# Optimization experiments

Hardware: AMD Instinct MI355X
Metric: run time of the kernel (lower is better)

The kernel has to match this reference:

```python
import jax, jax.numpy as jnp
import numpy as np
from jax import lax

NQ = 5  # qubits
NL = 3  # circuit layers


def conv2d(x, w, b):
    y = lax.conv_general_dilated(x, w, (1, 1), 'SAME',
                                 dimension_numbers=('NCHW', 'OIHW', 'NCHW'))
    return y + b[None, :, None, None]


def batchnorm(x, g, b, eps=1e-5):
    # training-mode batch statistics over (N,H,W), matching nn.BatchNorm2d in train()
    mu = x.mean((0, 2, 3), keepdims=True)
    var = x.var((0, 2, 3), keepdims=True)
    return g[None, :, None, None] * (x - mu) * lax.rsqrt(var + eps) + b[None, :, None, None]


def maxpool2(x):
    return lax.reduce_window(x, -jnp.inf, lax.max, (1, 1, 2, 2), (1, 1, 2, 2), 'VALID')


def _apply_1q(state, U, w):
    # state: (2,)*NQ, wire w is axis w (PennyLane default.qubit ordering)
    s = jnp.tensordot(U, state, axes=([1], [w]))
    return jnp.moveaxis(s, 0, w)


def _cnot(state, c, t):
    s0 = jnp.take(state, 0, axis=c)
    s1 = jnp.take(state, 1, axis=c)
    ta = t if t < c else t - 1
    s1 = jnp.flip(s1, axis=ta)  # X on target when control=1
    return jnp.stack([s0, s1], axis=c)


def _rx(t):
    c, s = jnp.cos(t / 2), jnp.sin(t / 2)
    return jnp.array([[c, -1j * s], [-1j * s, c]], dtype=jnp.complex64)


def _ry(t):
    c, s = jnp.cos(t / 2), jnp.sin(t / 2)
    return jnp.array([[c, -s], [s, c]], dtype=jnp.complex64)


def _rz(t):
    e = jnp.exp(-1j * t / 2)
    z = jnp.zeros((), jnp.complex64)
    return jnp.array([[e, z], [z, jnp.conj(e)]], dtype=jnp.complex64)


def quantum_circuit(inputs, weights):
    # inputs: (5,), weights: (30,)  -> scalar <Z0 Z1 Z2>
    state = jnp.zeros((2,) * NQ, jnp.complex64).at[(0,) * NQ].set(1.0)
    npl = NQ * 2  # weights per layer = 10
    nw = weights.shape[0]
    for l in range(NL):
        for i in range(NQ):
            state = _apply_1q(state, _rx(inputs[i]), i)
        for i in range(NQ):
            state = _apply_1q(state, _ry(weights[(l * npl + i) % nw]), i)
            state = _apply_1q(state, _rz(weights[(l * npl + i + NQ) % nw]), i)
        for i in range(NQ - 1):
            state = _cnot(state, i, i + 1)
        state = _cnot(state, NQ - 1, 0)
    probs = jnp.abs(state) ** 2
    z = jnp.array([1.0, -1.0], jnp.float32)
    sign = z[:, None, None] * z[None, :, None] * z[None, None, :]  # Z on wires 0,1,2
    return jnp.sum(probs * sign[:, :, :, None, None])


def setup_inputs() -> dict:
    key = jax.random.key(0)
    ks = jax.random.split(key, 12)
    d = {}
    d['x'] = jax.random.normal(ks[0], (256, 1, 224, 224), jnp.float32)
    d['conv1_w'] = jax.random.normal(ks[1], (16, 1, 3, 3), jnp.float32) * 0.1
    d['conv1_b'] = jnp.zeros((16,), jnp.float32)
    d['bn1_g'] = jnp.ones((16,), jnp.float32)
    d['bn1_b'] = jnp.zeros((16,), jnp.float32)
    d['conv2_w'] = jax.random.normal(ks[2], (32, 16, 3, 3), jnp.float32) * 0.05
    d['conv2_b'] = jnp.zeros((32,), jnp.float32)
    d['bn2_g'] = jnp.ones((32,), jnp.float32)
    d['bn2_b'] = jnp.zeros((32,), jnp.float32)
    d['conv3_w'] = jax.random.normal(ks[3], (64, 32, 3, 3), jnp.float32) * 0.05
    d['conv3_b'] = jnp.zeros((64,), jnp.float32)
    d['bn3_g'] = jnp.ones((64,), jnp.float32)
    d['bn3_b'] = jnp.zeros((64,), jnp.float32)
    d['fc1_w'] = jax.random.normal(ks[4], (64, 5), jnp.float32) * 0.1   # (in,out)
    d['fc1_b'] = jnp.zeros((5,), jnp.float32)
    d['ln_g'] = jnp.ones((5,), jnp.float32)
    d['ln_b'] = jnp.zeros((5,), jnp.float32)
    d['q_params'] = jax.random.uniform(ks[5], (30,), jnp.float32)
    d['fc2_w'] = jax.random.normal(ks[6], (1, 32), jnp.float32) * 0.5
    d['fc2_b'] = jnp.zeros((32,), jnp.float32)
    d['fc3_w'] = jax.random.normal(ks[7], (32, 2), jnp.float32) * 0.2
    d['fc3_b'] = jnp.zeros((2,), jnp.float32)
    return d


def reference(x, conv1_w, conv1_b, bn1_g, bn1_b, conv2_w, conv2_b, bn2_g, bn2_b,
              conv3_w, conv3_b, bn3_g, bn3_b, fc1_w, fc1_b, ln_g, ln_b,
              q_params, fc2_w, fc2_b, fc3_w, fc3_b):
    h = maxpool2(jax.nn.relu(batchnorm(conv2d(x, conv1_w, conv1_b), bn1_g, bn1_b)))
    h = maxpool2(jax.nn.relu(batchnorm(conv2d(h, conv2_w, conv2_b), bn2_g, bn2_b)))
    h = maxpool2(jax.nn.relu(batchnorm(conv2d(h, conv3_w, conv3_b), bn3_g, bn3_b)))
    # dropout is identity in eval; adaptive avg pool (1,1) + flatten
    h = h.mean((2, 3))                    # (B, 64)
    h = h @ fc1_w + fc1_b                 # (B, 5)
    mu = h.mean(-1, keepdims=True)
    var = h.var(-1, keepdims=True)
    h = ln_g * (h - mu) * lax.rsqrt(var + 1e-5) + ln_b
    q = jax.vmap(lambda inp: quantum_circuit(inp, q_params))(h)  # (B,)
    q = q[:, None].astype(jnp.float32)    # (B, 1)
    h2 = jax.nn.relu(q @ fc2_w + fc2_b)   # (B, 32)
    logits = h2 @ fc3_w + fc3_b           # (B, 2)
    return jax.nn.log_softmax(logits, axis=1)
```

## Files before the change

kernel.cpp:

```cpp
#include <hip/hip_runtime.h>
#include <hip/hip_bf16.h>


typedef _Float16 f16;
typedef _Float16 f16x2 __attribute__((ext_vector_type(2)));
typedef _Float16 f16x4 __attribute__((ext_vector_type(4)));
typedef _Float16 f16x8 __attribute__((ext_vector_type(8)));
typedef float f32x4 __attribute__((ext_vector_type(4)));
typedef float f32x16 __attribute__((ext_vector_type(16)));

#define DEV static __device__ __forceinline__

DEV float wave_sum(float v) {
#pragma unroll
  for (int off = 32; off > 0; off >>= 1) v += __shfl_xor(v, off, 64);
  return v;
}

__global__ __launch_bounds__(256) void repack(const float* __restrict__ w2,
                                              const float* __restrict__ w3,
                                              f16* __restrict__ Bt2,
                                              f16* __restrict__ Bt3) {
  int t = blockIdx.x * 256 + threadIdx.x;
  int T = gridDim.x * 256;
  for (int i = t; i < 32 * 168; i += T) {
    int oc = i / 168, kk = i - oc * 168;
    float v = 0.f;
    if (kk < 144) {
      int tap = kk >> 4, ic = kk & 15;
      v = w2[(oc * 16 + ic) * 9 + tap];
    }
    Bt2[i] = (f16)v;
  }
  for (int i = t; i < 64 * 296; i += T) {
    int oc = i / 296, kk = i - oc * 296;
    float v = 0.f;
    if (kk < 288) {
      int tap = kk / 32, ic = kk & 31;
      v = w3[(oc * 32 + ic) * 9 + tap];
    }
    Bt3[i] = (f16)v;
  }
}

__global__ __launch_bounds__(64) void finalize(const float* __restrict__ banks,
                                               const float* __restrict__ g,
                                               const float* __restrict__ b,
                                               float* __restrict__ scsh, int C,
                                               float inv_n) {
  int c = blockIdx.x, bk = threadIdx.x;
  float s = banks[bk * 2 * C + c];
  float qq = banks[bk * 2 * C + C + c];
  s = wave_sum(s);
  qq = wave_sum(qq);
  if (bk == 0) {
    float mean = s * inv_n;
    float var = qq * inv_n - mean * mean;
    float sc = g[c] * rsqrtf(var + 1e-5f);
    scsh[c] = sc;
    scsh[C + c] = b[c] - mean * sc;
  }
}

__global__ __launch_bounds__(256) void l1_mfma32(const float* __restrict__ x,
                                                 const float* __restrict__ w1,
                                                 float* __restrict__ banks,
                                                 f16* __restrict__ h1raw) {
  __shared__ f16 xA[18 * 240];
  __shared__ f16 xB[18 * 240];
  __shared__ f16 lrow[4 * 3616];
  __shared__ float lstat[32];
  int bid = blockIdx.x;
  int n = bid / 14, band = bid - n * 14;
  int y0 = band * 16;
  int t = threadIdx.x;
  if (t < 32) lstat[t] = 0.f;
  for (int i = t; i < 1008; i += 256) {
    int r = i / 56, k = i - r * 56;
    int y = y0 - 1 + r;
    float4 v = make_float4(0.f, 0.f, 0.f, 0.f);
    if ((unsigned)y < 224u)
      v = *(const float4*)(x + ((size_t)(n * 224 + y)) * 224 + k * 4);
    f16 h0 = (f16)v.x, h1 = (f16)v.y, h2 = (f16)v.z, h3 = (f16)v.w;
    f16* pa = xA + r * 240 + 4 * k + 1;
    pa[0] = h0; pa[1] = h1; pa[2] = h2; pa[3] = h3;
    f16x4 pk = {h0, h1, h2, h3};
    *(f16x4*)(xB + r * 240 + 4 * k) = pk;
  }
  if (t < 18) {
    xA[t * 240 + 0] = (f16)0.f;
    xA[t * 240 + 225] = (f16)0.f;
    xA[t * 240 + 226] = (f16)0.f;
    xB[t * 240 + 224] = (f16)0.f;
    xB[t * 240 + 225] = (f16)0.f;
  }
  __syncthreads();

  int wave = t >> 6, lane = t & 63;
  int g = lane >> 5, m32 = lane & 31;
  int oc = m32 & 15, s = m32 >> 4;

  f16x8 b;
#pragma unroll
  for (int j = 0; j < 8; j++) {
    int ky = 2 * g + (j >> 2), kx = j & 3;
    int kys = ky - s;
    float wv = 0.f;
    if (kx < 3 && kys >= 0 && kys < 3) wv = w1[oc * 9 + kys * 3 + kx];
    b[j] = (f16)wv;
  }

  const f16* abase = (m32 & 1) ? (xB + (m32 - 1)) : (xA + m32);
  f16* myrow = lrow + wave * 3616;
  f16* mrow = myrow + s * 1808;
  f32x16 zero16;
#pragma unroll
  for (int r = 0; r < 16; r++) zero16[r] = 0.f;
  const int bp[8] = {0, 1, 4, 5, 8, 9, 12, 13};
  float ssum = 0.f, ssq = 0.f;

  for (int rp = wave; rp < 8; rp += 4) {
    int r0 = 2 * rp + 2 * g;
    const f16* rbase = abase + r0 * 240;
#pragma unroll
    for (int xt = 0; xt < 7; xt++) {
      const f16* p0 = rbase + xt * 32;
      f16x2 v0 = *(const f16x2*)(p0);
      f16x2 v1 = *(const f16x2*)(p0 + 2);
      f16x2 v2 = *(const f16x2*)(p0 + 240);
      f16x2 v3 = *(const f16x2*)(p0 + 242);
      f16x8 a = {v0[0], v0[1], v1[0], v1[1], v2[0], v2[1], v3[0], v3[1]};
      f32x16 acc = __builtin_amdgcn_mfma_f32_32x32x16_f16(a, b, zero16, 0, 0, 0);
#pragma unroll
      for (int r = 0; r < 16; r++) {
        float v = acc[r];
        ssum += v;
        ssq += v * v;
      }
#pragma unroll
      for (int i = 0; i < 8; i++) {
        float pm = fmaxf(acc[2 * i], acc[2 * i + 1]);
        int pxp = xt * 16 + bp[i] + 2 * g;
        mrow[pxp * 16 + oc] = (f16)pm;
      }
    }
    int ph = band * 8 + rp;
    f16* gdst = h1raw + ((size_t)(n * 112) + ph) * 112 * 16;
    for (int i = lane; i < 224; i += 64) {
      f16x8 va = *(const f16x8*)(myrow + i * 8);
      f16x8 vb = *(const f16x8*)(myrow + 1808 + i * 8);
#pragma unroll
      for (int k = 0; k < 8; k++) va[k] = (va[k] > vb[k]) ? va[k] : vb[k];
      *(f16x8*)(gdst + i * 8) = va;
    }
  }
  ssum += __shfl_xor(ssum, 16, 64);
  ssum += __shfl_xor(ssum, 32, 64);
  ssq += __shfl_xor(ssq, 16, 64);
  ssq += __shfl_xor(ssq, 32, 64);
  if (lane < 16) {
    atomicAdd(&lstat[oc], ssum);
    atomicAdd(&lstat[16 + oc], ssq);
  }
  __syncthreads();
  if (t < 32) atomicAdd(&banks[(bid & 63) * 32 + t], lstat[t]);
}

__global__ __launch_bounds__(256) void l2_gemm(const f16* __restrict__ h1,
                                               const f16* __restrict__ Btg,
                                               const float* __restrict__ scsh1,
                                               f16* __restrict__ p2,
                                               float* __restrict__ banks) {
  extern __shared__ char smem[];
  f16* lin = (f16*)smem;
  float* lstat = (float*)(smem + 32832);
  f16* lpool = (f16*)smem;
  int bid = blockIdx.x;
  int n = bid / 28, band = bid - n * 28, h0 = band * 4;
  int t = threadIdx.x;
  int wave = t >> 6, lane = t & 63, q = lane >> 4, wi = lane & 15;
  const int icq = (q & 1) * 8;
  f16x8 breg0[5], breg1[5];
#pragma unroll
  for (int j = 0; j < 5; j++) {
    breg0[j] = *(const f16x8*)(Btg + wi * 168 + j * 32 + q * 8);
    breg1[j] = *(const f16x8*)(Btg + (16 + wi) * 168 + j * 32 + q * 8);
  }
  if (t < 64) lstat[t] = 0.f;
  {
    for (int i = t; i < 1344; i += 256) {
      int r = i / 224, c = i - r * 224;
      int y = h0 + r - 1;
      f16x8 o = {0, 0, 0, 0, 0, 0, 0, 0};
      if ((unsigned)y < 112u) {
        f16x8 xv =
            *(const f16x8*)(h1 + ((size_t)(n * 112 + y)) * 112 * 16 + c * 8);
        int ch0 = (c & 1) * 8;
#pragma unroll
        for (int k = 0; k < 8; k++) {
          float f = (float)xv[k] * scsh1[ch0 + k] + scsh1[16 + ch0 + k];
          o[k] = (f16)fmaxf(f, 0.f);
        }
      }
      *(f16x8*)(lin + (r * 114 + 1 + (c >> 1)) * 24 + (c & 1) * 8) = o;
    }
    if (t < 24) {
      int r = t >> 2, k = t & 3;
      f16x8 z = {0, 0, 0, 0, 0, 0, 0, 0};
      int pos = (k < 2) ? 0 : 113;
      *(f16x8*)(lin + (r * 114 + pos) * 24 + (k & 1) * 8) = z;
    }
  }
  __syncthreads();
  f32x4 acc[7][2];
#pragma unroll
  for (int f = 0; f < 7; f++)
#pragma unroll
    for (int nf = 0; nf < 2; nf++)
#pragma unroll
      for (int r = 0; r < 4; r++) acc[f][nf][r] = 0.f;

#pragma unroll
  for (int j = 0; j < 5; j++) {
    const int tA = 2 * j, tB = 2 * j + 1;
    const int kyA = tA / 3, kxA = tA % 3;
    const int kyB = (tB < 9) ? tB / 3 : 0, kxB = (tB < 9) ? tB % 3 : 0;
    bool hiq = (q >= 2);
    int ky = hiq ? kyB : kyA;
    int kx = hiq ? kxB : kxA;
    const f16* aptr0 = lin + ((wave + ky) * 114 + wi + kx) * 24 + icq;
    f16x8 b0 = breg0[j];
    f16x8 b1 = breg1[j];
#pragma unroll
    for (int f = 0; f < 7; f++) {
      f16x8 a = *(const f16x8*)(aptr0 + f * 384);
      acc[f][0] = __builtin_amdgcn_mfma_f32_16x16x32_f16(a, b0, acc[f][0], 0, 0, 0);
      acc[f][1] = __builtin_amdgcn_mfma_f32_16x16x32_f16(a, b1, acc[f][1], 0, 0, 0);
    }
  }
  float s0 = 0.f, q0 = 0.f, s1 = 0.f, q1 = 0.f;
#pragma unroll
  for (int f = 0; f < 7; f++)
#pragma unroll
    for (int r = 0; r < 4; r++) {
      float v0 = acc[f][0][r], v1 = acc[f][1][r];
      s0 += v0; q0 += v0 * v0;
      s1 += v1; q1 += v1 * v1;
    }
  s0 += __shfl_xor(s0, 16, 64); s0 += __shfl_xor(s0, 32, 64);
  q0 += __shfl_xor(q0, 16, 64); q0 += __shfl_xor(q0, 32, 64);
  s1 += __shfl_xor(s1, 16, 64); s1 += __shfl_xor(s1, 32, 64);
  q1 += __shfl_xor(q1, 16, 64); q1 += __shfl_xor(q1, 32, 64);
  if (q == 0) {
    atomicAdd(&lstat[wi], s0);
    atomicAdd(&lstat[16 + wi], s1);
    atomicAdd(&lstat[32 + wi], q0);
    atomicAdd(&lstat[48 + wi], q1);
  }
  __syncthreads();
  if (wave & 1) {
#pragma unroll
    for (int f = 0; f < 7; f++)
#pragma unroll
      for (int nf = 0; nf < 2; nf++) {
        int ch = nf * 16 + wi;
        int pc0 = f * 8 + q * 2;
        float m0 = fmaxf(acc[f][nf][0], acc[f][nf][1]);
        float m1 = fmaxf(acc[f][nf][2], acc[f][nf][3]);
        lpool[((wave >> 1) * 56 + pc0) * 32 + ch] = (f16)m0;
        lpool[((wave >> 1) * 56 + pc0 + 1) * 32 + ch] = (f16)m1;
      }
  }
  __syncthreads();
  if (!(wave & 1)) {
    int ph = band * 2 + (wave >> 1);
#pragma unroll
    for (int f = 0; f < 7; f++)
#pragma unroll
      for (int nf = 0; nf < 2; nf++) {
        int ch = nf * 16 + wi;
        int pc0 = f * 8 + q * 2;
        float m0 = fmaxf(acc[f][nf][0], acc[f][nf][1]);
        float m1 = fmaxf(acc[f][nf][2], acc[f][nf][3]);
        m0 = fmaxf(m0, (float)lpool[((wave >> 1) * 56 + pc0) * 32 + ch]);
        m1 = fmaxf(m1, (float)lpool[((wave >> 1) * 56 + pc0 + 1) * 32 + ch]);
        size_t ob = (((size_t)n * 56 + ph) * 56) * 32;
        p2[ob + (size_t)pc0 * 32 + ch] = (f16)m0;
        p2[ob + (size_t)(pc0 + 1) * 32 + ch] = (f16)m1;
      }
  }
  if (t < 64) {
    int i = t >> 5, c = t & 31;
    atomicAdd(&banks[(bid & 63) * 64 + i * 32 + c], lstat[i * 32 + c]);
  }
}

__global__ __launch_bounds__(256) void l3_gemm(const f16* __restrict__ p2,
                                               const f16* __restrict__ Btg,
                                               const float* __restrict__ scsh2,
                                               f16* __restrict__ p3,
                                               float* __restrict__ banks) {
  extern __shared__ char smem[];
  f16* lin = (f16*)smem;
  float* lstat = (float*)(smem + 27840);
  f16* lpool = (f16*)smem;
  int bx = blockIdx.x;
  int n = bx / 14, band = bx - n * 14, h0 = band * 4;
  int t = threadIdx.x;
  int wave = t >> 6, lane = t & 63, q = lane >> 4, wi = lane & 15;
  int mhalf = wave & 1, nfpair = wave >> 1;
  f16x8 breg0[9], breg1[9];
#pragma unroll
  for (int j = 0; j < 9; j++) {
    breg0[j] = *(const f16x8*)(Btg + (nfpair * 32 + wi) * 296 + j * 32 + q * 8);
    breg1[j] =
        *(const f16x8*)(Btg + (nfpair * 32 + 16 + wi) * 296 + j * 32 + q * 8);
  }
  if (t < 128) lstat[t] = 0.f;
  {
    for (int i = t; i < 1344; i += 256) {
      int r = i / 224, rem = i - r * 224;
      int c = rem >> 2, cp = rem & 3;
      int y = h0 + r - 1;
      f16x8 o = {0, 0, 0, 0, 0, 0, 0, 0};
      if ((unsigned)y < 56u) {
        const f16* src = p2 + (((size_t)(n * 56 + y)) * 56 + c) * 32 + cp * 8;
        f16x8 xv = *(const f16x8*)src;
        int ch0 = cp * 8;
#pragma unroll
        for (int k = 0; k < 8; k++) {
          float f = (float)xv[k] * scsh2[ch0 + k] + scsh2[32 + ch0 + k];
          o[k] = (f16)fmaxf(f, 0.f);
        }
      }
      *(f16x8*)(lin + (r * 58 + 1 + c) * 40 + cp * 8) = o;
    }
    if (t < 48) {
      int r = t / 8, k = t & 7;
      int col = (k < 4) ? 0 : 57, cp = k & 3;
      f16x8 z = {0, 0, 0, 0, 0, 0, 0, 0};
      *(f16x8*)(lin + (r * 58 + col) * 40 + cp * 8) = z;
    }
  }
  __syncthreads();
  int abase[7];
#pragma unroll
  for (int f = 0; f < 7; f++) {
    int pos = mhalf * 112 + f * 16 + wi;
    int r = pos / 56, w = pos - r * 56;
    abase[f] = (r * 58 + w) * 40 + q * 8;
  }
  f32x4 acc[7][2];
#pragma unroll
  for (int f = 0; f < 7; f++)
#pragma unroll
    for (int nf = 0; nf < 2; nf++)
#pragma unroll
      for (int r = 0; r < 4; r++) acc[f][nf][r] = 0.f;

#pragma unroll
  for (int j = 0; j < 9; j++) {
    const int ky = j / 3, kx = j % 3;
    f16x8 b0 = breg0[j];
    f16x8 b1 = breg1[j];
#pragma unroll
    for (int f = 0; f < 7; f++) {
      f16x8 a = *(const f16x8*)(lin + abase[f] + (ky * 58 + kx) * 40);
      acc[f][0] = __builtin_amdgcn_mfma_f32_16x16x32_f16(a, b0, acc[f][0], 0, 0, 0);
      acc[f][1] = __builtin_amdgcn_mfma_f32_16x16x32_f16(a, b1, acc[f][1], 0, 0, 0);
    }
  }
  int ch0 = nfpair * 32 + wi, ch1 = ch0 + 16;
  float s0 = 0.f, q0 = 0.f, s1 = 0.f, q1 = 0.f;
#pragma unroll
  for (int f = 0; f < 7; f++)
#pragma unroll
    for (int r = 0; r < 4; r++) {
      float v0 = acc[f][0][r], v1 = acc[f][1][r];
      s0 += v0; q0 += v0 * v0;
      s1 += v1; q1 += v1 * v1;
    }
  s0 += __shfl_xor(s0, 16, 64); s0 += __shfl_xor(s0, 32, 64);
  q0 += __shfl_xor(q0, 16, 64); q0 += __shfl_xor(q0, 32, 64);
  s1 += __shfl_xor(s1, 16, 64); s1 += __shfl_xor(s1, 32, 64);
  q1 += __shfl_xor(q1, 16, 64); q1 += __shfl_xor(q1, 32, 64);
  if (q == 0) {
    atomicAdd(&lstat[ch0], s0);
    atomicAdd(&lstat[ch1], s1);
    atomicAdd(&lstat[64 + ch0], q0);
    atomicAdd(&lstat[64 + ch1], q1);
  }
  __syncthreads();
#pragma unroll
  for (int f = 0; f < 7; f++) {
    int pos = mhalf * 112 + f * 16 + q * 4;
    int r0 = pos / 56, w0 = pos - r0 * 56;
#pragma unroll
    for (int nf = 0; nf < 2; nf++) {
      int ch = nf ? ch1 : ch0;
      float m0 = fmaxf(acc[f][nf][0], acc[f][nf][1]);
      float m1 = fmaxf(acc[f][nf][2], acc[f][nf][3]);
      lpool[(r0 * 28 + (w0 >> 1)) * 64 + ch] = (f16)m0;
      lpool[(r0 * 28 + (w0 >> 1) + 1) * 64 + ch] = (f16)m1;
    }
  }
  __syncthreads();
  for (int i = t; i < 3584; i += 256) {
    int ch = i & 63, rest = i >> 6;
    int pc = rest % 28, pr = rest / 28;
    float v = fmaxf((float)lpool[((2 * pr) * 28 + pc) * 64 + ch],
                    (float)lpool[((2 * pr + 1) * 28 + pc) * 64 + ch]);
    int gpr = band * 2 + pr;
    p3[(((size_t)n * 28 + gpr) * 28 + pc) * 64 + ch] = (f16)v;
  }
  if (t < 128) {
    atomicAdd(&banks[(bx & 63) * 128 + t], lstat[t]);
  }
}

__global__ __launch_bounds__(256) void head_pool(
    const f16* __restrict__ p3, const float* __restrict__ scsh3,
    const float* __restrict__ fc1w, const float* __restrict__ fc1b,
    float* __restrict__ featg) {
  int n = blockIdx.x, t = threadIdx.x;
  __shared__ float red[64 * 33];
  __shared__ float meanc[64];
  int oct = t & 7, strip = t >> 3;
  float sc[8], sh[8];
#pragma unroll
  for (int k = 0; k < 8; k++) {
    sc[k] = scsh3[oct * 8 + k];
    sh[k] = scsh3[64 + oct * 8 + k];
  }
  float acc[8];
#pragma unroll
  for (int k = 0; k < 8; k++) acc[k] = 0.f;
  const f16* base = p3 + (size_t)n * 50176 + oct * 8;
  for (int px = strip; px < 784; px += 32) {
    f16x8 v = *(const f16x8*)(base + (size_t)px * 64);
#pragma unroll
    for (int k = 0; k < 8; k++)
      acc[k] += fmaxf((float)v[k] * sc[k] + sh[k], 0.f);
  }
#pragma unroll
  for (int k = 0; k < 8; k++) red[(oct * 8 + k) * 33 + strip] = acc[k];
  __syncthreads();
  if (t < 64) {
    float s = 0.f;
    for (int j = 0; j < 32; j++) s += red[t * 33 + j];
    meanc[t] = s * (1.f / 784.f);
  }
  __syncthreads();
  if (t < 5) {
    float a = fc1b[t];
    for (int i = 0; i < 64; i++) a += meanc[i] * fc1w[i * 5 + t];
    featg[n * 8 + t] = a;
  }
}

template <int W>
DEV void g_rx(float (&sr)[32], float (&si)[32], float c, float s) {
  constexpr int m = 1 << (4 - W);
#pragma unroll
  for (int i0 = 0; i0 < 32; i0++)
    if (!(i0 & m)) {
      int i1 = i0 | m;
      float a0r = sr[i0], a0i = si[i0], a1r = sr[i1], a1i = si[i1];
      sr[i0] = c * a0r + s * a1i;
      si[i0] = c * a0i - s * a1r;
      sr[i1] = s * a0i + c * a1r;
      si[i1] = -s * a0r + c * a1i;
    }
}

template <int W>
DEV void g_ry(float (&sr)[32], float (&si)[32], float c, float s) {
  constexpr int m = 1 << (4 - W);
#pragma unroll
  for (int i0 = 0; i0 < 32; i0++)
    if (!(i0 & m)) {
      int i1 = i0 | m;
      float a0r = sr[i0], a0i = si[i0], a1r = sr[i1], a1i = si[i1];
      sr[i0] = c * a0r - s * a1r;
      si[i0] = c * a0i - s * a1i;
      sr[i1] = s * a0r + c * a1r;
      si[i1] = s * a0i + c * a1i;
    }
}

template <int W>
DEV void g_rz(float (&sr)[32], float (&si)[32], float c, float s) {
  constexpr int m = 1 << (4 - W);
#pragma unroll
  for (int i0 = 0; i0 < 32; i0++)
    if (!(i0 & m)) {
      int i1 = i0 | m;
      float a0r = sr[i0], a0i = si[i0], a1r = sr[i1], a1i = si[i1];
      sr[i0] = c * a0r + s * a0i;
      si[i0] = c * a0i - s * a0r;
      sr[i1] = c * a1r - s * a1i;
      si[i1] = c * a1i + s * a1r;
    }
}

template <int C, int T>
DEV void g_cnot(float (&sr)[32], float (&si)[32]) {
  constexpr int mc = 1 << (4 - C), mt = 1 << (4 - T);
#pragma unroll
  for (int i0 = 0; i0 < 32; i0++)
    if ((i0 & mc) && !(i0 & mt)) {
      int i1 = i0 | mt;
      float tr = sr[i0]; sr[i0] = sr[i1]; sr[i1] = tr;
      float ti = si[i0]; si[i0] = si[i1]; si[i1] = ti;
    }
}

__global__ __launch_bounds__(64) void head_q(
    const float* __restrict__ featg, const float* __restrict__ lng,
    const float* __restrict__ lnb, const float* __restrict__ qp,
    const float* __restrict__ fc2w, const float* __restrict__ fc2b,
    const float* __restrict__ fc3w, const float* __restrict__ fc3b,
    float* __restrict__ out) {
  int n = blockIdx.x * 64 + threadIdx.x;
  float f[5];
#pragma unroll
  for (int i = 0; i < 5; i++) f[i] = featg[n * 8 + i];
  float mu = (f[0] + f[1] + f[2] + f[3] + f[4]) * 0.2f;
  float var = 0.f;
#pragma unroll
  for (int i = 0; i < 5; i++) { float d = f[i] - mu; var += d * d; }
  var *= 0.2f;
  float inv = rsqrtf(var + 1e-5f);
#pragma unroll
  for (int i = 0; i < 5; i++) f[i] = lng[i] * (f[i] - mu) * inv + lnb[i];

  float cx[5], sx[5];
#pragma unroll
  for (int i = 0; i < 5; i++) {
    cx[i] = cosf(0.5f * f[i]);
    sx[i] = sinf(0.5f * f[i]);
  }
  float sr[32], si[32];
#pragma unroll
  for (int i = 0; i < 32; i++) { sr[i] = 0.f; si[i] = 0.f; }
  sr[0] = 1.f;

  for (int l = 0; l < 3; l++) {
    g_rx<0>(sr, si, cx[0], sx[0]);
    g_rx<1>(sr, si, cx[1], sx[1]);
    g_rx<2>(sr, si, cx[2], sx[2]);
    g_rx<3>(sr, si, cx[3], sx[3]);
    g_rx<4>(sr, si, cx[4], sx[4]);
#define WIRE_YZ(I)                                             \
  {                                                            \
    float ty = qp[l * 10 + I];                                 \
    g_ry<I>(sr, si, cosf(0.5f * ty), sinf(0.5f * ty));         \
    float tz = qp[l * 10 + I + 5];                             \
    g_rz<I>(sr, si, cosf(0.5f * tz), sinf(0.5f * tz));         \
  }
    WIRE_YZ(0) WIRE_YZ(1) WIRE_YZ(2) WIRE_YZ(3) WIRE_YZ(4)
#undef WIRE_YZ
    g_cnot<0, 1>(sr, si);
    g_cnot<1, 2>(sr, si);
    g_cnot<2, 3>(sr, si);
    g_cnot<3, 4>(sr, si);
    g_cnot<4, 0>(sr, si);
  }
  float qv = 0.f;
#pragma unroll
  for (int idx = 0; idx < 32; idx++) {
    float p = sr[idx] * sr[idx] + si[idx] * si[idx];
    qv += (__popc(idx & 0x1C) & 1) ? -p : p;
  }
  float l0 = fc3b[0], l1 = fc3b[1];
  for (int j = 0; j < 32; j++) {
    float hv = fmaxf(qv * fc2w[j] + fc2b[j], 0.f);
    l0 += hv * fc3w[j * 2];
    l1 += hv * fc3w[j * 2 + 1];
  }
  float mx = fmaxf(l0, l1);
  float lse = mx + logf(expf(l0 - mx) + expf(l1 - mx));
  out[n * 2 + 0] = l0 - lse;
  out[n * 2 + 1] = l1 - lse;
}

extern "C" void kernel_launch(void* const* d_in, const int* in_sizes, int n_in,
                              void* d_out, int out_size, void* d_ws,
                              size_t ws_size, hipStream_t stream) {
  const float* x    = (const float*)d_in[0];
  const float* w1   = (const float*)d_in[1];
  const float* bn1g = (const float*)d_in[3];
  const float* bn1b = (const float*)d_in[4];
  const float* w2   = (const float*)d_in[5];
  const float* bn2g = (const float*)d_in[7];
  const float* bn2b = (const float*)d_in[8];
  const float* w3   = (const float*)d_in[9];
  const float* bn3g = (const float*)d_in[11];
  const float* bn3b = (const float*)d_in[12];
  const float* fc1w = (const float*)d_in[13];
  const float* fc1b = (const float*)d_in[14];
  const float* lng  = (const float*)d_in[15];
  const float* lnb  = (const float*)d_in[16];
  const float* qp   = (const float*)d_in[17];
  const float* fc2w = (const float*)d_in[18];
  const float* fc2b = (const float*)d_in[19];
  const float* fc3w = (const float*)d_in[20];
  const float* fc3b = (const float*)d_in[21];
  float* out = (float*)d_out;

  char* ws = (char*)d_ws;
  float* banks1 = (float*)ws;
  float* banks2 = (float*)(ws + 8192);
  float* banks3 = (float*)(ws + 24576);
  float* scsh1 = (float*)(ws + 57344);
  float* scsh2 = (float*)(ws + 57472);
  float* scsh3 = (float*)(ws + 57728);
  f16* Bt2 = (f16*)(ws + 58240);
  f16* Bt3 = (f16*)(ws + 68992);
  f16* h1 = (f16*)(ws + 106880);
  f16* p2 = (f16*)(ws + 106880 + 102760448ULL);
  f16* p3 = (f16*)(ws + 106880 + 102760448ULL + 51380224ULL);
  float* featg = banks2;

  hipMemsetAsync(ws, 0, 57344, stream);
  repack<<<16, 256, 0, stream>>>(w2, w3, Bt2, Bt3);
  l1_mfma32<<<3584, 256, 0, stream>>>(x, w1, banks1, h1);
  finalize<<<16, 64, 0, stream>>>(banks1, bn1g, bn1b, scsh1, 16,
                                  1.f / 12845056.f);
  l2_gemm<<<7168, 256, 33088, stream>>>(h1, Bt2, scsh1, p2, banks2);
  finalize<<<32, 64, 0, stream>>>(banks2, bn2g, bn2b, scsh2, 32,
                                  1.f / 3211264.f);
  l3_gemm<<<3584, 256, 28352, stream>>>(p2, Bt3, scsh2, p3, banks3);
  finalize<<<64, 64, 0, stream>>>(banks3, bn3g, bn3b, scsh3, 64,
                                  1.f / 802816.f);
  head_pool<<<256, 256, 0, stream>>>(p3, scsh3, fc1w, fc1b, featg);
  head_q<<<4, 64, 0, stream>>>(featg, lng, lnb, qp, fc2w, fc2b, fc3w, fc3b,
                               out);
}
```

Baseline: 367.2 us.

## Make l2_gemm persistent over four bands with double-buffered LDS prefetch

Each l2_gemm block now handles four consecutive 4-row bands instead of one, cutting the grid from 7168 to 1792 blocks. The block prefetches the next band's input into registers and writes it to a second LDS buffer while the current band's MFMAs run. BN statistics accumulate across bands before one atomic flush, which reduces per-block setup, B-fragment loads and atomics. The cost is higher LDS use (about 73KB) and register pressure under launch_bounds(256,2), which lowers occupancy, and one extra barrier per band.

```diff
diff --git a/kernel.cpp b/kernel.cpp
--- a/kernel.cpp
+++ b/kernel.cpp
@@ -166,129 +166,211 @@
   if (t < 32) atomicAdd(&banks[(bid & 63) * 32 + t], lstat[t]);
 }
 
-__global__ __launch_bounds__(256) void l2_gemm(const f16* __restrict__ h1,
-                                               const f16* __restrict__ Btg,
-                                               const float* __restrict__ scsh1,
-                                               f16* __restrict__ p2,
-                                               float* __restrict__ banks) {
+__global__ __launch_bounds__(256, 2) void l2_gemm(
+    const f16* __restrict__ h1, const f16* __restrict__ Btg,
+    const float* __restrict__ scsh1, f16* __restrict__ p2,
+    float* __restrict__ banks) {
   extern __shared__ char smem[];
-  f16* lin = (f16*)smem;
-  float* lstat = (float*)(smem + 32832);
-  f16* lpool = (f16*)smem;
+  f16* lin0 = (f16*)smem;
+  f16* lin1 = (f16*)(smem + 32832);
+  f16* lpool = (f16*)(smem + 65664);
+  float* lstat = (float*)(smem + 72832);
   int bid = blockIdx.x;
-  int n = bid / 28, band = bid - n * 28, h0 = band * 4;
+  int n = bid / 7, sb = bid - n * 7;
   int t = threadIdx.x;
   int wave = t >> 6, lane = t & 63, q = lane >> 4, wi = lane & 15;
   const int icq = (q & 1) * 8;
+
   f16x8 breg0[5], breg1[5];
 #pragma unroll
   for (int j = 0; j < 5; j++) {
     breg0[j] = *(const f16x8*)(Btg + wi * 168 + j * 32 + q * 8);
     breg1[j] = *(const f16x8*)(Btg + (16 + wi) * 168 + j * 32 + q * 8);
   }
+
+  f16x8 L[6];
+  {
+    int gb4 = sb * 16;
+#pragma unroll
+    for (int k = 0; k < 6; k++) {
+      int i = t + k * 256;
+      f16x8 v = {0, 0, 0, 0, 0, 0, 0, 0};
+      if (i < 1344) {
+        int r = i / 224, c = i - r * 224;
+        int y = gb4 + r - 1;
+        if ((unsigned)y < 112u)
+          v = *(const f16x8*)(h1 + ((size_t)(n * 112 + y)) * 112 * 16 + c * 8);
+      }
+      L[k] = v;
+    }
+  }
+  __builtin_amdgcn_sched_barrier(0);
   if (t < 64) lstat[t] = 0.f;
+  if (t < 48) {
+    f16* dst = (t < 24) ? lin0 : lin1;
+    int tt = (t < 24) ? t : t - 24;
+    int r = tt >> 2, k2 = tt & 3;
+    f16x8 z = {0, 0, 0, 0, 0, 0, 0, 0};
+    int pos = (k2 < 2) ? 0 : 113;
+    *(f16x8*)(dst + (r * 114 + pos) * 24 + (k2 & 1) * 8) = z;
+  }
   {
-    for (int i = t; i < 1344; i += 256) {
-      int r = i / 224, c = i - r * 224;
-      int y = h0 + r - 1;
-      f16x8 o = {0, 0, 0, 0, 0, 0, 0, 0};
-      if ((unsigned)y < 112u) {
-        f16x8 xv =
-            *(const f16x8*)(h1 + ((size_t)(n * 112 + y)) * 112 * 16 + c * 8);
-        int ch0 = (c & 1) * 8;
-#pragma unroll
-        for (int k = 0; k < 8; k++) {
-          float f = (float)xv[k] * scsh1[ch0 + k] + scsh1[16 + ch0 + k];
-          o[k] = (f16)fmaxf(f, 0.f);
+    int gb4 = sb * 16;
+#pragma unroll
+    for (int k = 0; k < 6; k++) {
+      int i = t + k * 256;
+      if (i < 1344) {
+        int r = i / 224, c = i - r * 224;
+        int y = gb4 + r - 1;
+        f16x8 o = {0, 0, 0, 0, 0, 0, 0, 0};
+        if ((unsigned)y < 112u) {
+          f16x8 xv = L[k];
+          int ch0 = (c & 1) * 8;
+#pragma unroll
+          for (int e = 0; e < 8; e++) {
+            float f = (float)xv[e] * scsh1[ch0 + e] + scsh1[16 + ch0 + e];
+            o[e] = (f16)fmaxf(f, 0.f);
+          }
         }
-      }
-      *(f16x8*)(lin + (r * 114 + 1 + (c >> 1)) * 24 + (c & 1) * 8) = o;
-    }
-    if (t < 24) {
-      int r = t >> 2, k = t & 3;
-      f16x8 z = {0, 0, 0, 0, 0, 0, 0, 0};
-      int pos = (k < 2) ? 0 : 113;
-      *(f16x8*)(lin + (r * 114 + pos) * 24 + (k & 1) * 8) = z;
-    }
-  }
-  __syncthreads();
-  f32x4 acc[7][2];
-#pragma unroll
-  for (int f = 0; f < 7; f++)
-#pragma unroll
-    for (int nf = 0; nf < 2; nf++)
-#pragma unroll
-      for (int r = 0; r < 4; r++) acc[f][nf][r] = 0.f;
-
-#pragma unroll
-  for (int j = 0; j < 5; j++) {
-    const int tA = 2 * j, tB = 2 * j + 1;
-    const int kyA = tA / 3, kxA = tA % 3;
-    const int kyB = (tB < 9) ? tB / 3 : 0, kxB = (tB < 9) ? tB % 3 : 0;
-    bool hiq = (q >= 2);
-    int ky = hiq ? kyB : kyA;
-    int kx = hiq ? kxB : kxA;
-    const f16* aptr0 = lin + ((wave + ky) * 114 + wi + kx) * 24 + icq;
-    f16x8 b0 = breg0[j];
-    f16x8 b1 = breg1[j];
-#pragma unroll
-    for (int f = 0; f < 7; f++) {
-      f16x8 a = *(const f16x8*)(aptr0 + f * 384);
-      acc[f][0] = __builtin_amdgcn_mfma_f32_16x16x32_f16(a, b0, acc[f][0], 0, 0, 0);
-      acc[f][1] = __builtin_amdgcn_mfma_f32_16x16x32_f16(a, b1, acc[f][1], 0, 0, 0);
-    }
-  }
-  float s0 = 0.f, q0 = 0.f, s1 = 0.f, q1 = 0.f;
-#pragma unroll
-  for (int f = 0; f < 7; f++)
-#pragma unroll
-    for (int r = 0; r < 4; r++) {
-      float v0 = acc[f][0][r], v1 = acc[f][1][r];
-      s0 += v0; q0 += v0 * v0;
-      s1 += v1; q1 += v1 * v1;
-    }
-  s0 += __shfl_xor(s0, 16, 64); s0 += __shfl_xor(s0, 32, 64);
-  q0 += __shfl_xor(q0, 16, 64); q0 += __shfl_xor(q0, 32, 64);
-  s1 += __shfl_xor(s1, 16, 64); s1 += __shfl_xor(s1, 32, 64);
-  q1 += __shfl_xor(q1, 16, 64); q1 += __shfl_xor(q1, 32, 64);
+        *(f16x8*)(lin0 + (r * 114 + 1 + (c >> 1)) * 24 + (c & 1) * 8) = o;
+      }
+    }
+  }
+  __syncthreads();
+
+  float tS0 = 0.f, tQ0 = 0.f, tS1 = 0.f, tQ1 = 0.f;
+  f16* cur = lin0;
+  f16* nxt = lin1;
+
+  for (int b = 0; b < 4; b++) {
+    int gb = sb * 4 + b;
+    if (b < 3) {
+      int gb4 = (gb + 1) * 4;
+#pragma unroll
+      for (int k = 0; k < 6; k++) {
+        int i = t + k * 256;
+        f16x8 v = {0, 0, 0, 0, 0, 0, 0, 0};
+        if (i < 1344) {
+          int r = i / 224, c = i - r * 224;
+          int y = gb4 + r - 1;
+          if ((unsigned)y < 112u)
+            v = *(const f16x8*)(h1 +
+                                ((size_t)(n * 112 + y)) * 112 * 16 + c * 8);
+        }
+        L[k] = v;
+      }
+      __builtin_amdgcn_sched_barrier(0);
+    }
+
+    f32x4 acc[7][2];
+#pragma unroll
+    for (int f = 0; f < 7; f++)
+#pragma unroll
+      for (int nf = 0; nf < 2; nf++)
+#pragma unroll
+        for (int r = 0; r < 4; r++) acc[f][nf][r] = 0.f;
+
+#pragma unroll
+    for (int j = 0; j < 5; j++) {
+      const int tA = 2 * j, tB = 2 * j + 1;
+      const int kyA = tA / 3, kxA = tA % 3;
+      const int kyB = (tB < 9) ? tB / 3 : 0, kxB = (tB < 9) ? tB % 3 : 0;
+      bool hiq = (q >= 2);
+      int ky = hiq ? kyB : kyA;
+      int kx = hiq ? kxB : kxA;
+      const f16* aptr0 = cur + ((wave + ky) * 114 + wi + kx) * 24 + icq;
+      f16x8 b0 = breg0[j];
+      f16x8 b1 = breg1[j];
+#pragma unroll
+      for (int f = 0; f < 7; f++) {
+        f16x8 a = *(const f16x8*)(aptr0 + f * 384);
+        acc[f][0] =
+            __builtin_amdgcn_mfma_f32_16x16x32_f16(a, b0, acc[f][0], 0, 0, 0);
+        acc[f][1] =
+            __builtin_amdgcn_mfma_f32_16x16x32_f16(a, b1, acc[f][1], 0, 0, 0);
+      }
+    }
+
+#pragma unroll
+    for (int f = 0; f < 7; f++)
+#pragma unroll
+      for (int r = 0; r < 4; r++) {
+        float v0 = acc[f][0][r], v1 = acc[f][1][r];
+        tS0 += v0; tQ0 += v0 * v0;
+        tS1 += v1; tQ1 += v1 * v1;
+      }
+
+    if (wave & 1) {
+#pragma unroll
+      for (int f = 0; f < 7; f++)
+#pragma unroll
+        for (int nf = 0; nf < 2; nf++) {
+          int ch = nf * 16 + wi;
+          int pc0 = f * 8 + q * 2;
+          float m0 = fmaxf(acc[f][nf][0], acc[f][nf][1]);
+          float m1 = fmaxf(acc[f][nf][2], acc[f][nf][3]);
+          lpool[((wave >> 1) * 56 + pc0) * 32 + ch] = (f16)m0;
+          lpool[((wave >> 1) * 56 + pc0 + 1) * 32 + ch] = (f16)m1;
+        }
+    }
+
+    if (b < 3) {
+      int gb4 = (gb + 1) * 4;
+#pragma unroll
+      for (int k = 0; k < 6; k++) {
+        int i = t + k * 256;
+        if (i < 1344) {
+          int r = i / 224, c = i - r * 224;
+          int y = gb4 + r - 1;
+          f16x8 o = {0, 0, 0, 0, 0, 0, 0, 0};
+          if ((unsigned)y < 112u) {
+            f16x8 xv = L[k];
+            int ch0 = (c & 1) * 8;
+#pragma unroll
+            for (int e = 0; e < 8; e++) {
+              float f = (float)xv[e] * scsh1[ch0 + e] + scsh1[16 + ch0 + e];
+              o[e] = (f16)fmaxf(f, 0.f);
+            }
+          }
+          *(f16x8*)(nxt + (r * 114 + 1 + (c >> 1)) * 24 + (c & 1) * 8) = o;
+        }
+      }
+    }
+    __syncthreads();
+
+    if (!(wave & 1)) {
+      int ph = gb * 2 + (wave >> 1);
+#pragma unroll
+      for (int f = 0; f < 7; f++)
+#pragma unroll
+        for (int nf = 0; nf < 2; nf++) {
+          int ch = nf * 16 + wi;
+          int pc0 = f * 8 + q * 2;
+          float m0 = fmaxf(acc[f][nf][0], acc[f][nf][1]);
+          float m1 = fmaxf(acc[f][nf][2], acc[f][nf][3]);
+          m0 = fmaxf(m0, (float)lpool[((wave >> 1) * 56 + pc0) * 32 + ch]);
+          m1 = fmaxf(m1, (float)lpool[((wave >> 1) * 56 + pc0 + 1) * 32 + ch]);
+          size_t ob = (((size_t)n * 56 + ph) * 56) * 32;
+          p2[ob + (size_t)pc0 * 32 + ch] = (f16)m0;
+          p2[ob + (size_t)(pc0 + 1) * 32 + ch] = (f16)m1;
+        }
+    }
+    __syncthreads();
+
+    f16* tmpp = cur; cur = nxt; nxt = tmpp;
+  }
+
+  tS0 += __shfl_xor(tS0, 16, 64); tS0 += __shfl_xor(tS0, 32, 64);
+  tQ0 += __shfl_xor(tQ0, 16, 64); tQ0 += __shfl_xor(tQ0, 32, 64);
+  tS1 += __shfl_xor(tS1, 16, 64); tS1 += __shfl_xor(tS1, 32, 64);
+  tQ1 += __shfl_xor(tQ1, 16, 64); tQ1 += __shfl_xor(tQ1, 32, 64);
   if (q == 0) {
-    atomicAdd(&lstat[wi], s0);
-    atomicAdd(&lstat[16 + wi], s1);
-    atomicAdd(&lstat[32 + wi], q0);
-    atomicAdd(&lstat[48 + wi], q1);
-  }
-  __syncthreads();
-  if (wave & 1) {
-#pragma unroll
-    for (int f = 0; f < 7; f++)
-#pragma unroll
-      for (int nf = 0; nf < 2; nf++) {
-        int ch = nf * 16 + wi;
-        int pc0 = f * 8 + q * 2;
-        float m0 = fmaxf(acc[f][nf][0], acc[f][nf][1]);
-        float m1 = fmaxf(acc[f][nf][2], acc[f][nf][3]);
-        lpool[((wave >> 1) * 56 + pc0) * 32 + ch] = (f16)m0;
-        lpool[((wave >> 1) * 56 + pc0 + 1) * 32 + ch] = (f16)m1;
-      }
-  }
-  __syncthreads();
-  if (!(wave & 1)) {
-    int ph = band * 2 + (wave >> 1);
-#pragma unroll
-    for (int f = 0; f < 7; f++)
-#pragma unroll
-      for (int nf = 0; nf < 2; nf++) {
-        int ch = nf * 16 + wi;
-        int pc0 = f * 8 + q * 2;
-        float m0 = fmaxf(acc[f][nf][0], acc[f][nf][1]);
-        float m1 = fmaxf(acc[f][nf][2], acc[f][nf][3]);
-        m0 = fmaxf(m0, (float)lpool[((wave >> 1) * 56 + pc0) * 32 + ch]);
-        m1 = fmaxf(m1, (float)lpool[((wave >> 1) * 56 + pc0 + 1) * 32 + ch]);
-        size_t ob = (((size_t)n * 56 + ph) * 56) * 32;
-        p2[ob + (size_t)pc0 * 32 + ch] = (f16)m0;
-        p2[ob + (size_t)(pc0 + 1) * 32 + ch] = (f16)m1;
-      }
-  }
+    atomicAdd(&lstat[wi], tS0);
+    atomicAdd(&lstat[16 + wi], tS1);
+    atomicAdd(&lstat[32 + wi], tQ0);
+    atomicAdd(&lstat[48 + wi], tQ1);
+  }
+  __syncthreads();
   if (t < 64) {
     int i = t >> 5, c = t & 31;
     atomicAdd(&banks[(bid & 63) * 64 + i * 32 + c], lstat[i * 32 + c]);
@@ -627,7 +709,7 @@
   l1_mfma32<<<3584, 256, 0, stream>>>(x, w1, banks1, h1);
   finalize<<<16, 64, 0, stream>>>(banks1, bn1g, bn1b, scsh1, 16,
                                   1.f / 12845056.f);
-  l2_gemm<<<7168, 256, 33088, stream>>>(h1, Bt2, scsh1, p2, banks2);
+  l2_gemm<<<1792, 256, 73088, stream>>>(h1, Bt2, scsh1, p2, banks2);
   finalize<<<32, 64, 0, stream>>>(banks2, bn2g, bn2b, scsh2, 32,
                                   1.f / 3211264.f);
   l3_gemm<<<3584, 256, 28352, stream>>>(p2, Bt3, scsh2, p3, banks3);
```

Result: faster. 357.8 us (-2.6%).
